# Kernel optimization log

Measured on AMD Instinct MI355X. Metric: run time of the kernel, lower is better.

## Reference

```python
import jax, jax.numpy as jnp
import numpy as np

# Dims
B, C, D, H, W = 2, 64, 16, 64, 64
G = 2            # deformable groups (choose_group(64, 2) -> 2)
K = 27           # 3x3x3 kernel points
GC = C // G      # channels per group
AXIS = (0.5, 1.0, 1.0)   # offset_axis_scale (d, h, w)
EPS = 1e-5
# kernel point offsets for k=3, pad=1, dilation=1: {-1,0,1}^3
_KOFF = np.array([(a, b, c) for a in (-1, 0, 1) for b in (-1, 0, 1) for c in (-1, 0, 1)], dtype=np.float32)


def conv3d(x, w, b=None, pad=0):
    y = jax.lax.conv_general_dilated(x, w, (1, 1, 1), [(pad, pad)] * 3,
                                     dimension_numbers=('NCDHW', 'OIDHW', 'NCDHW'))
    if b is not None:
        y = y + b[None, :, None, None, None]
    return y


def proj1x1(x, w, b=None):
    y = jnp.einsum('oc,bcdhw->bodhw', w, x)
    if b is not None:
        y = y + b[None, :, None, None, None]
    return y


def _trilinear_sample(vflat, pd, ph, pw):
    # vflat: [B,G,GC,DHW]; pd/ph/pw: [B,G,DHW] float sampling coords; zeros padding outside
    d0 = jnp.floor(pd); h0 = jnp.floor(ph); w0 = jnp.floor(pw)
    td, th, tw = pd - d0, ph - h0, pw - w0
    d0 = d0.astype(jnp.int32); h0 = h0.astype(jnp.int32); w0 = w0.astype(jnp.int32)
    acc = jnp.zeros_like(vflat)
    for dd in (0, 1):
        for hh in (0, 1):
            for ww in (0, 1):
                di, hi, wi = d0 + dd, h0 + hh, w0 + ww
                valid = ((di >= 0) & (di < D) & (hi >= 0) & (hi < H) & (wi >= 0) & (wi < W)).astype(vflat.dtype)
                idx = (jnp.clip(di, 0, D - 1) * H + jnp.clip(hi, 0, H - 1)) * W + jnp.clip(wi, 0, W - 1)
                g = jnp.take_along_axis(vflat, jnp.broadcast_to(idx[:, :, None, :], vflat.shape), axis=3)
                wgt = ((td if dd else 1.0 - td) * (th if hh else 1.0 - th) * (tw if ww else 1.0 - tw)) * valid
                acc = acc + g * wgt[:, :, None, :]
    return acc


def setup_inputs() -> dict:
    key = jax.random.key(0)
    ks = jax.random.split(key, 8)
    f = jnp.float32
    s = 1.0 / np.sqrt(C)
    return {
        'x': jax.random.normal(ks[0], (B, C, D, H, W), f),
        'gate': jnp.zeros((), f),
        'pre_w': jax.random.normal(ks[1], (C, C, 1, 1, 1), f) * s,
        'post_w': jax.random.normal(ks[2], (C, C, 1, 1, 1), f) * s,
        'in_proj_w': jax.random.normal(ks[3], (C, C), f) * s,
        'in_proj_b': jnp.zeros((C,), f),
        'out_proj_w': jax.random.normal(ks[4], (C, C), f) * s,
        'out_proj_b': jnp.zeros((C,), f),
        'off_w': jax.random.normal(ks[5], (3 * G * K, C, 3, 3, 3), f) * 0.01,
        'off_b': jnp.zeros((3 * G * K,), f),
        'mask_w': jax.random.normal(ks[6], (G * K, C, 3, 3, 3), f) * 0.01,
        'mask_b': jnp.zeros((G * K,), f),
        'in_gamma': jnp.ones((C,), f),
        'in_beta': jnp.zeros((C,), f),
    }


def reference(x, gate, pre_w, post_w, in_proj_w, in_proj_b, out_proj_w, out_proj_b,
              off_w, off_b, mask_w, mask_b, in_gamma, in_beta):
    DHW = D * H * W
    xp = conv3d(x, pre_w)                                      # pre 1x1
    # --- DCNv3_3D: value projection, learned offsets + softmax modulation mask ---
    v = proj1x1(xp, in_proj_w, in_proj_b).reshape(B, G, GC, DHW)
    off = conv3d(xp, off_w, off_b, pad=1).reshape(B, G, K, 3, DHW)   # warmed-up offset_scale = 1.0
    m = jax.nn.softmax(conv3d(xp, mask_w, mask_b, pad=1).reshape(B, G, K, DHW), axis=2)
    dg, hg, wg = jnp.meshgrid(jnp.arange(D, dtype=jnp.float32),
                              jnp.arange(H, dtype=jnp.float32),
                              jnp.arange(W, dtype=jnp.float32), indexing='ij')
    dg, hg, wg = dg.reshape(-1), hg.reshape(-1), wg.reshape(-1)      # [DHW]
    out = jnp.zeros_like(v)
    for k in range(K):   # fixed small loop over 27 kernel points
        pd = dg + _KOFF[k, 0] + off[:, :, k, 0] * AXIS[0]
        ph = hg + _KOFF[k, 1] + off[:, :, k, 1] * AXIS[1]
        pw = wg + _KOFF[k, 2] + off[:, :, k, 2] * AXIS[2]
        out = out + _trilinear_sample(v, pd, ph, pw) * m[:, :, k, :][:, :, None, :]
    y = out.reshape(B, C, D, H, W)
    y = proj1x1(y, out_proj_w, out_proj_b)
    # InstanceNorm3d + GELU
    mu = y.mean(axis=(2, 3, 4), keepdims=True)
    var = y.var(axis=(2, 3, 4), keepdims=True)
    y = (y - mu) * jax.lax.rsqrt(var + EPS)
    y = y * in_gamma[None, :, None, None, None] + in_beta[None, :, None, None, None]
    y = jax.nn.gelu(y)
    y = conv3d(y, post_w)                                      # post 1x1
    return x + jax.nn.sigmoid(gate) * y
```

## Files before the change

### kernel.cpp

```cpp
#include <hip/hip_runtime.h>
#include <hip/hip_bf16.h>

typedef short short8 __attribute__((ext_vector_type(8)));
typedef float f32x4 __attribute__((ext_vector_type(4)));
typedef _Float16 h2 __attribute__((ext_vector_type(2)));
typedef __fp16 fp16x2 __attribute__((ext_vector_type(2)));

#if __has_builtin(__builtin_elementwise_fma)
#define FMA2H(a, b, c) __builtin_elementwise_fma((a), (b), (c))
#else
#define FMA2H(a, b, c) ((a) * (b) + (c))
#endif

namespace {
constexpr int Bn = 2, Cn = 64, Dn = 16, Hn = 64, Wn = 64;
constexpr int Gn = 2, Kn = 27, GCn = 32;
constexpr int DHW = Dn * Hn * Wn;
constexpr int OCn = 216;
constexpr int PD = 18, PH = 66, PW = 66;
constexpr float EPS = 1e-5f;

constexpr int PROWS = 12 * 66;
constexpr int PATCH_B = PROWS * 128;

constexpr size_t XPADH_OFF = 0;
constexpr size_t XPADH_B   = (size_t)Bn * PD * PH * PW * Cn * 2;
constexpr size_t WFRAG_OFF = XPADH_OFF + XPADH_B;
constexpr size_t WFRAG_B   = (size_t)54 * 16 * 64 * 16;
constexpr size_t WV_OFF    = WFRAG_OFF + WFRAG_B;
constexpr size_t WV_B      = 64 * 64 * 4;
constexpr size_t CONV_OFF  = WV_OFF + WV_B;
constexpr size_t CONV_B    = (size_t)Bn * OCn * DHW * 2;
constexpr size_t V_OFF     = CONV_OFF + CONV_B;
constexpr size_t V_B       = (size_t)Bn * Gn * DHW * GCn * 2;
constexpr size_t SAMP_OFF  = V_OFF + V_B;
constexpr size_t SAMP_B    = (size_t)Bn * Gn * DHW * GCn * 2;
constexpr size_t STAT_OFF  = SAMP_OFF + SAMP_B;
constexpr size_t VBH_OFF   = STAT_OFF + 4096;
constexpr size_t VFRAG_OFF = VBH_OFF + 256;
constexpr size_t OFRAG_OFF = VFRAG_OFF + 8192;
constexpr size_t PFRAG_OFF = OFRAG_OFF + 8192;
}

__device__ inline float b2f(short s) {
  union { float f; unsigned u; } x; x.u = ((unsigned)(unsigned short)s) << 16; return x.f;
}
__device__ inline short f2b(float f) {
  __hip_bfloat16 h = __float2bfloat16(f);
  union { __hip_bfloat16 h; short s; } x; x.h = h; return x.s;
}
__device__ inline int iclamp(int v, int lo, int hi) { return v < lo ? lo : (v > hi ? hi : v); }
__device__ inline h2 u2h2(unsigned u) {
  union { unsigned u; h2 h; } x; x.u = u; return x.h;
}
__device__ inline unsigned h2u(h2 h) {
  union { unsigned u; h2 h; } x; x.h = h; return x.u;
}
__device__ inline h2 pkrtz(float a, float b) {
#if __has_builtin(__builtin_amdgcn_cvt_pkrtz)
  union { fp16x2 p; h2 h; } x;
  x.p = __builtin_amdgcn_cvt_pkrtz(a, b);
  return x.h;
#else
  return (h2){(_Float16)a, (_Float16)b};
#endif
}

__global__ __launch_bounds__(256) void zerofill(uint4* __restrict__ p, int n16) {
  int i = blockIdx.x * 256 + threadIdx.x;
  if (i < n16) p[i] = make_uint4(0, 0, 0, 0);
}

__global__ __launch_bounds__(256) void fillpad(const float* __restrict__ x,
                                               __hip_bfloat16* __restrict__ xpadh) {
  int tid = threadIdx.x;
  int w5 = tid & 31, cq = tid >> 5;
  int p = blockIdx.x * 32 + w5;
  int b = blockIdx.y;
  int w = p & 63, h = (p >> 6) & 63, d = p >> 12;
  const float* xb = x + ((size_t)b * 64 + cq * 8) * DHW + p;
  short8 o8;
#pragma unroll
  for (int j = 0; j < 8; ++j) o8[j] = f2b(xb[(size_t)j * DHW]);
  __hip_bfloat16* ob = xpadh + (size_t)b * (PD * PH * PW * 64)
      + ((((size_t)(d + 1) * 66) + (h + 1)) * 66 + (w + 1)) * 64 + cq * 8;
  *(short8*)ob = o8;
}

__global__ __launch_bounds__(256) void fold_weights(
    const float* __restrict__ pre_w, const float* __restrict__ in_proj_w,
    const float* __restrict__ off_w, const float* __restrict__ mask_w,
    short8* __restrict__ Wfrag, float* __restrict__ Wv) {
  int i = blockIdx.x * 256 + threadIdx.x;
  if (i < 64 * 64) {
    int o = i >> 6, c = i & 63;
    float s = 0.f;
    for (int cp = 0; cp < 64; ++cp) s += in_proj_w[o * 64 + cp] * pre_w[cp * 64 + c];
    Wv[i] = s;
    return;
  }
  int t = i - 64 * 64;
  if (t >= 54 * 16 * 64) return;
  int l = t & 63; int rest = t >> 6;
  int mt = rest & 15; int ks = rest >> 4;
  int oc = mt * 16 + (l & 15);
  int tap = ks >> 1;
  int c0 = (ks & 1) * 32 + (l >> 4) * 8;
  float vals[8] = {0.f, 0.f, 0.f, 0.f, 0.f, 0.f, 0.f, 0.f};
  if (oc < OCn) {
    const float* cw = (oc < 162) ? (off_w + (size_t)oc * 64 * 27)
                                 : (mask_w + (size_t)(oc - 162) * 64 * 27);
#pragma unroll 1
    for (int cp = 0; cp < 64; ++cp) {
      float wv = cw[cp * 27 + tap];
      const float* pr = pre_w + cp * 64 + c0;
#pragma unroll
      for (int j = 0; j < 8; ++j) vals[j] += wv * pr[j];
    }
  }
  short8 o8;
#pragma unroll
  for (int j = 0; j < 8; ++j) o8[j] = f2b(vals[j]);
  Wfrag[t] = o8;
}

__global__ __launch_bounds__(256) void packfrag(
    const float* __restrict__ Wv, const float* __restrict__ Wout,
    const float* __restrict__ Wpost, const float* __restrict__ vb,
    short8* __restrict__ vfrag, short8* __restrict__ ofrag,
    short8* __restrict__ pfrag, h2* __restrict__ vbh) {
  int i = blockIdx.x * 256 + threadIdx.x;
  if (i < 32) vbh[i] = pkrtz(vb[2 * i], vb[2 * i + 1]);
  int which = i >> 9;
  int t = i & 511;
  int l = t & 63, mt = (t >> 6) & 3, ks = t >> 8;
  int m = mt * 16 + (l & 15);
  int k0 = ks * 32 + (l >> 4) * 8;
  const float* W = (which == 0) ? Wv : (which == 1) ? Wout : Wpost;
  short8 o;
#pragma unroll
  for (int j = 0; j < 8; ++j) o[j] = f2b(W[m * 64 + k0 + j]);
  if (which == 0) vfrag[t] = o;
  else if (which == 1) ofrag[t] = o;
  else pfrag[t] = o;
}

#define GEMM_MFMA_BODY(FRAG)                                                  \
  int wid = tid >> 6, l = tid & 63, lm = l & 15, lk = l >> 4;                 \
  f32x4 acc[4][4];                                                            \
  _Pragma("unroll")                                                           \
  for (int mt = 0; mt < 4; ++mt)                                              \
    _Pragma("unroll")                                                         \
    for (int nt = 0; nt < 4; ++nt) acc[mt][nt] = (f32x4){0.f, 0.f, 0.f, 0.f}; \
  _Pragma("unroll")                                                           \
  for (int ks = 0; ks < 2; ++ks) {                                            \
    short8 af[4], bf[4];                                                      \
    _Pragma("unroll")                                                         \
    for (int mt = 0; mt < 4; ++mt) af[mt] = FRAG[(ks * 4 + mt) * 64 + l];     \
    _Pragma("unroll")                                                         \
    for (int nt = 0; nt < 4; ++nt) {                                          \
      int sr = wid * 64 + nt * 16 + lm;                                       \
      int us = ks * 4 + lk;                                                   \
      bf[nt] = *(const short8*)(stg + sr * 128 + ((us ^ (sr & 7)) << 4));     \
    }                                                                         \
    _Pragma("unroll")                                                         \
    for (int mt = 0; mt < 4; ++mt)                                            \
      _Pragma("unroll")                                                       \
      for (int nt = 0; nt < 4; ++nt)                                          \
        acc[mt][nt] = __builtin_amdgcn_mfma_f32_16x16x32_bf16(af[mt], bf[nt], acc[mt][nt], 0, 0, 0); \
  }

__global__ __launch_bounds__(256) void vproj_mfma(
    const char* __restrict__ xpadh, const short8* __restrict__ vfrag,
    const h2* __restrict__ vbh, _Float16* __restrict__ v) {
  __shared__ char stg[32768];
  __shared__ char bnc[256 * 144];
  int tid = threadIdx.x;
  int p0 = blockIdx.x * 256, b = blockIdx.y;
  const char* xb = xpadh + (size_t)b * (PD * PH * PW * 128);
#pragma unroll
  for (int it = 0; it < 8; ++it) {
    int idx = it * 256 + tid;
    int s = idx >> 3, slot = idx & 7;
    int p = p0 + s, w = p & 63, h = (p >> 6) & 63, d = p >> 12;
    const char* g = xb + ((((size_t)(d + 1)) * 66 + (h + 1)) * 66 + (w + 1)) * 128 + slot * 16;
    *(uint4*)(stg + s * 128 + ((slot ^ (s & 7)) << 4)) = *(const uint4*)g;
  }
  __syncthreads();
  GEMM_MFMA_BODY(vfrag)
#pragma unroll
  for (int mt = 0; mt < 4; ++mt)
#pragma unroll
    for (int nt = 0; nt < 4; ++nt)
#pragma unroll
      for (int r = 0; r < 4; ++r) {
        int pos = wid * 64 + nt * 16 + lm;
        int oc = mt * 16 + lk * 4 + r;
        *(_Float16*)(bnc + pos * 144 + oc * 2) = (_Float16)acc[mt][nt][r];
      }
  __syncthreads();
  {
    int p = p0 + tid;
    const unsigned* brow = (const unsigned*)(bnc + tid * 144);
    char* vb0 = (char*)v + ((size_t)(b * 2 + 0) * DHW + p) * 64;
    char* vb1 = (char*)v + ((size_t)(b * 2 + 1) * DHW + p) * 64;
#pragma unroll
    for (int s = 0; s < 8; ++s) {
      uint4 ov;
      unsigned* po = (unsigned*)&ov;
#pragma unroll
      for (int j = 0; j < 4; ++j) {
        h2 hv = u2h2(brow[s * 4 + j]) + vbh[s * 4 + j];
        po[j] = h2u(hv);
      }
      if (s < 4) *(uint4*)(vb0 + s * 16) = ov;
      else       *(uint4*)(vb1 + (s - 4) * 16) = ov;
    }
  }
}

__global__ __launch_bounds__(512) void conv_mfma(
    const char* __restrict__ xpadh, const char* __restrict__ wfrag,
    const float* __restrict__ off_b, const float* __restrict__ mask_b,
    __hip_bfloat16* __restrict__ convout) {
  __shared__ char lds[PATCH_B];
  int tid = threadIdx.x;
  int h0 = blockIdx.x * 2, d = blockIdx.y, b = blockIdx.z;

  const char* xb = xpadh + (size_t)b * (PD * PH * PW * 128);
  for (int idx = tid; idx < PROWS * 8; idx += 512) {
    int s = idx >> 3, slot = idx & 7;
    int r12 = s / 66, wx = s - r12 * 66;
    int dp = r12 >> 2, hp = r12 & 3;
    const char* g = xb + ((((size_t)(d + dp)) * 66 + (h0 + hp)) * 66 + wx) * 128 + slot * 16;
    *(uint4*)(lds + s * 128 + ((slot ^ (s & 7)) << 4)) = *(const uint4*)g;
  }
  __syncthreads();

  int wid = tid >> 6, l = tid & 63;
  int wm = wid & 3, wn = wid >> 2;
  int lm = l & 15, lk = l >> 4;
  const char* abase = wfrag + ((size_t)((wm * 4) * 64 + l)) * 16;

  f32x4 acc[4][4];
#pragma unroll
  for (int mt = 0; mt < 4; ++mt)
#pragma unroll
    for (int nt = 0; nt < 4; ++nt) acc[mt][nt] = (f32x4){0.f, 0.f, 0.f, 0.f};

  short8 A0[4], B0[4], A1[4], B1[4], A2[4], B2[4];

#define LOADA(KS, A)                                                          \
  {                                                                           \
    const char* ap_ = abase + (KS) * 16384;                                   \
    _Pragma("unroll")                                                         \
    for (int mt = 0; mt < 4; ++mt) A[mt] = *(const short8*)(ap_ + mt * 1024); \
  }
#define LOADB(KS, B)                                                          \
  {                                                                           \
    int tap_ = (KS) >> 1;                                                     \
    int dd_ = tap_ / 9, rem_ = tap_ - dd_ * 9;                                \
    int dh_ = rem_ / 3, dw_ = rem_ - dh_ * 3;                                 \
    int srow_ = (dd_ * 4 + wn + dh_) * 66 + dw_;                              \
    int uslot_ = 4 * ((KS) & 1) + lk;                                         \
    _Pragma("unroll")                                                         \
    for (int nt = 0; nt < 4; ++nt) {                                          \
      int sr_ = srow_ + nt * 16 + lm;                                         \
      B[nt] = *(const short8*)(lds + sr_ * 128 + ((uslot_ ^ (sr_ & 7)) << 4)); \
    }                                                                         \
  }
#define MFMAS(A, B)                                                           \
  __builtin_amdgcn_s_setprio(1);                                              \
  _Pragma("unroll")                                                           \
  for (int mt = 0; mt < 4; ++mt)                                              \
    _Pragma("unroll")                                                         \
    for (int nt = 0; nt < 4; ++nt)                                            \
      acc[mt][nt] = __builtin_amdgcn_mfma_f32_16x16x32_bf16(A[mt], B[nt], acc[mt][nt], 0, 0, 0); \
  __builtin_amdgcn_s_setprio(0);

  LOADA(0, A0) LOADB(0, B0)
  LOADA(1, A1) LOADB(1, B1)
#pragma unroll 1
  for (int ks = 0; ks < 54; ks += 3) {
    LOADA(ks + 2, A2) LOADB(ks + 2, B2)
    MFMAS(A0, B0)
    if (ks + 3 < 54) { LOADA(ks + 3, A0) LOADB(ks + 3, B0) }
    MFMAS(A1, B1)
    if (ks + 4 < 54) { LOADA(ks + 4, A1) LOADB(ks + 4, B1) }
    MFMAS(A2, B2)
  }
#undef LOADA
#undef LOADB
#undef MFMAS

  int pbase = d * 4096 + (h0 + wn) * 64;
#pragma unroll
  for (int mt = 0; mt < 4; ++mt) {
    int oc0 = wm * 64 + mt * 16 + lk * 4;
#pragma unroll
    for (int r = 0; r < 4; ++r) {
      int oc = oc0 + r;
      if (oc < OCn) {
        float bias = (oc < 162) ? off_b[oc] : mask_b[oc - 162];
        size_t orow = ((size_t)b * OCn + oc) * DHW + pbase;
#pragma unroll
        for (int nt = 0; nt < 4; ++nt)
          convout[orow + nt * 16 + lm] = __float2bfloat16(acc[mt][nt][r] + bias);
      }
    }
  }
}

__global__ __launch_bounds__(256) void dcn_sample(
    const __hip_bfloat16* __restrict__ convout, const _Float16* __restrict__ v,
    short* __restrict__ sampled) {
  __shared__ short offm[108 * 64];
  int tid = threadIdx.x;
  int id = blockIdx.x;
  int bg = (id & 7) >> 1;
  int p0 = (((id >> 3) << 1) + (id & 1)) * 64;
  int b = bg >> 1, g = bg & 1;

  const __hip_bfloat16* cb = convout + (size_t)b * OCn * DHW;
#pragma unroll 1
  for (int idx = tid; idx < 108 * 8; idx += 256) {
    int row = idx >> 3, col = idx & 7;
    int oc = (row < 81) ? (g * 81 + row) : (162 + g * Kn + (row - 81));
    *(uint4*)(offm + row * 64 + col * 8) = *(const uint4*)(cb + (size_t)oc * DHW + p0 + col * 8);
  }
  __syncthreads();

  int pl = tid >> 2, q = tid & 3;
  int p = p0 + pl;
  int w = p & 63, h = (p >> 6) & 63, d = p >> 12;

  float msum = 0.f;
  h2 acc[4];
#pragma unroll
  for (int j = 0; j < 4; ++j) acc[j] = (h2){(_Float16)0.f, (_Float16)0.f};
  const char* vg = (const char*)v + ((size_t)bg * DHW * GCn + q * 8) * 2;

#pragma unroll 1
  for (int k = 0; k < Kn; ++k) {
    float offd = b2f(offm[(3 * k + 0) * 64 + pl]);
    float offh = b2f(offm[(3 * k + 1) * 64 + pl]);
    float offw = b2f(offm[(3 * k + 2) * 64 + pl]);
    float pd = (float)(d + (k / 9) - 1) + offd * 0.5f;
    float ph = (float)(h + ((k / 3) % 3) - 1) + offh;
    float pw = (float)(w + (k % 3) - 1) + offw;
    float fd = floorf(pd), fh = floorf(ph), fw = floorf(pw);
    float td = pd - fd, th = ph - fh, tw = pw - fw;
    int d0 = (int)fd, h0 = (int)fh, w0 = (int)fw;
    float ek = __expf(b2f(offm[(81 + k) * 64 + pl]));
    msum += ek;

    float wd0 = ((unsigned)d0 < (unsigned)Dn) ? (1.f - td) * ek : 0.f;
    float wd1 = ((unsigned)(d0 + 1) < (unsigned)Dn) ? td * ek : 0.f;
    float wh0 = ((unsigned)h0 < (unsigned)Hn) ? (1.f - th) : 0.f;
    float wh1 = ((unsigned)(h0 + 1) < (unsigned)Hn) ? th : 0.f;
    float ww0 = ((unsigned)w0 < (unsigned)Wn) ? (1.f - tw) : 0.f;
    float ww1 = ((unsigned)(w0 + 1) < (unsigned)Wn) ? tw : 0.f;
    int dr0 = iclamp(d0, 0, Dn - 1) << 18, dr1 = iclamp(d0 + 1, 0, Dn - 1) << 18;
    int hr0 = iclamp(h0, 0, Hn - 1) << 12, hr1 = iclamp(h0 + 1, 0, Hn - 1) << 12;
    int wc0 = iclamp(w0, 0, Wn - 1) << 6,  wc1 = iclamp(w0 + 1, 0, Wn - 1) << 6;
    float wdh00 = wd0 * wh0, wdh01 = wd0 * wh1, wdh10 = wd1 * wh0, wdh11 = wd1 * wh1;

#define CORNER(BOFF, WT)                                                \
    {                                                                   \
      _Float16 wh_ = (_Float16)(WT);                                    \
      h2 w2_ = {wh_, wh_};                                              \
      uint4 u_ = *(const uint4*)(vg + (BOFF));                          \
      acc[0] = FMA2H(u2h2(u_.x), w2_, acc[0]);                          \
      acc[1] = FMA2H(u2h2(u_.y), w2_, acc[1]);                          \
      acc[2] = FMA2H(u2h2(u_.z), w2_, acc[2]);                          \
      acc[3] = FMA2H(u2h2(u_.w), w2_, acc[3]);                          \
    }
    CORNER(dr0 + hr0 + wc0, wdh00 * ww0)
    CORNER(dr0 + hr0 + wc1, wdh00 * ww1)
    CORNER(dr0 + hr1 + wc0, wdh01 * ww0)
    CORNER(dr0 + hr1 + wc1, wdh01 * ww1)
    CORNER(dr1 + hr0 + wc0, wdh10 * ww0)
    CORNER(dr1 + hr0 + wc1, wdh10 * ww1)
    CORNER(dr1 + hr1 + wc0, wdh11 * ww0)
    CORNER(dr1 + hr1 + wc1, wdh11 * ww1)
#undef CORNER
  }

  float rs = 1.f / msum;
  short8 o8;
#pragma unroll
  for (int j = 0; j < 4; ++j) {
    o8[2 * j]     = f2b((float)acc[j][0] * rs);
    o8[2 * j + 1] = f2b((float)acc[j][1] * rs);
  }
  *(short8*)((char*)sampled + ((size_t)bg * DHW + p) * 64 + q * 16) = o8;
}

__global__ __launch_bounds__(256) void outproj_mfma(
    const short* __restrict__ sampled, const short8* __restrict__ ofrag,
    const float* __restrict__ ob, __hip_bfloat16* __restrict__ t) {
  __shared__ char stg[32768];
  __shared__ char bnc[256 * 144];
  int tid = threadIdx.x;
  int p0 = blockIdx.x * 256, b = blockIdx.y;
#pragma unroll
  for (int it = 0; it < 8; ++it) {
    int idx = it * 256 + tid;
    int s = idx >> 3, slot = idx & 7;
    int g = slot >> 2;
    const char* src = (const char*)sampled + ((size_t)(b * 2 + g) * DHW + p0 + s) * 64 + (slot & 3) * 16;
    *(uint4*)(stg + s * 128 + ((slot ^ (s & 7)) << 4)) = *(const uint4*)src;
  }
  __syncthreads();
  GEMM_MFMA_BODY(ofrag)
#pragma unroll
  for (int mt = 0; mt < 4; ++mt)
#pragma unroll
    for (int r = 0; r < 4; ++r) {
      int oc = mt * 16 + lk * 4 + r;
      float bias = ob[oc];
#pragma unroll
      for (int nt = 0; nt < 4; ++nt) {
        int pos = wid * 64 + nt * 16 + lm;
        *(short*)(bnc + pos * 144 + oc * 2) = f2b(acc[mt][nt][r] + bias);
      }
    }
  __syncthreads();
  {
    int c = tid & 63, pq = tid >> 6;
    short* trow = (short*)t + ((size_t)b * 64 + c) * DHW + p0 + pq * 64;
#pragma unroll
    for (int s8 = 0; s8 < 8; ++s8) {
      short8 o8;
#pragma unroll
      for (int j = 0; j < 8; ++j)
        o8[j] = *(const short*)(bnc + (pq * 64 + s8 * 8 + j) * 144 + c * 2);
      *(short8*)(trow + s8 * 8) = o8;
    }
  }
}

__global__ __launch_bounds__(256) void stats_k(const __hip_bfloat16* __restrict__ t,
                                               float* __restrict__ stat) {
  int bc = blockIdx.x;
  const short8* tc = (const short8*)(t + (size_t)bc * DHW);
  float s = 0.f, ss = 0.f;
  for (int i = threadIdx.x; i < DHW / 8; i += 256) {
    short8 s8 = tc[i];
#pragma unroll
    for (int j = 0; j < 8; ++j) { float xv = b2f(s8[j]); s += xv; ss += xv * xv; }
  }
#pragma unroll
  for (int o = 32; o > 0; o >>= 1) { s += __shfl_down(s, o); ss += __shfl_down(ss, o); }
  __shared__ float ls[4], lss[4];
  int wid = threadIdx.x >> 6;
  if ((threadIdx.x & 63) == 0) { ls[wid] = s; lss[wid] = ss; }
  __syncthreads();
  if (threadIdx.x == 0) {
    float S = ls[0] + ls[1] + ls[2] + ls[3];
    float SS = lss[0] + lss[1] + lss[2] + lss[3];
    float mu = S / (float)DHW;
    float var = SS / (float)DHW - mu * mu;
    stat[bc * 2 + 0] = mu;
    stat[bc * 2 + 1] = rsqrtf(var + EPS);
  }
}

__global__ __launch_bounds__(256) void normgelu(
    const __hip_bfloat16* __restrict__ t, const float* __restrict__ stat,
    const float* __restrict__ gamma, const float* __restrict__ beta,
    short* __restrict__ nvh) {
  int p = blockIdx.x * 256 + threadIdx.x;
  int b = blockIdx.y;
  short o[64];
#pragma unroll
  for (int c = 0; c < Cn; ++c) {
    float mu = stat[(b * Cn + c) * 2 + 0];
    float rstd = stat[(b * Cn + c) * 2 + 1];
    float tv = b2f(((const short*)t)[((size_t)b * Cn + c) * DHW + p]);
    float yv = (tv - mu) * rstd * gamma[c] + beta[c];
    float u = 0.7978845608028654f * (yv + 0.044715f * yv * yv * yv);
    float e = __expf(2.f * u);
    float th = 1.f - 2.f / (e + 1.f);
    o[c] = f2b(0.5f * yv * (1.f + th));
  }
  short* dst = nvh + ((size_t)b * DHW + p) * 64;
#pragma unroll
  for (int s8 = 0; s8 < 8; ++s8) {
    short8 o8;
#pragma unroll
    for (int j = 0; j < 8; ++j) o8[j] = o[s8 * 8 + j];
    *(short8*)(dst + s8 * 8) = o8;
  }
}

__global__ __launch_bounds__(256) void post_mfma(
    const short* __restrict__ nvh, const short8* __restrict__ pfrag,
    const float* __restrict__ x, const float* __restrict__ gate,
    float* __restrict__ out) {
  __shared__ char stg[32768];
  __shared__ char bnc[256 * 144];
  int tid = threadIdx.x;
  int p0 = blockIdx.x * 256, b = blockIdx.y;
#pragma unroll
  for (int it = 0; it < 8; ++it) {
    int idx = it * 256 + tid;
    int s = idx >> 3, slot = idx & 7;
    const char* src = (const char*)nvh + ((size_t)b * DHW + p0 + s) * 128 + slot * 16;
    *(uint4*)(stg + s * 128 + ((slot ^ (s & 7)) << 4)) = *(const uint4*)src;
  }
  __syncthreads();
  GEMM_MFMA_BODY(pfrag)
#pragma unroll
  for (int mt = 0; mt < 4; ++mt)
#pragma unroll
    for (int nt = 0; nt < 4; ++nt)
#pragma unroll
      for (int r = 0; r < 4; ++r) {
        int pos = wid * 64 + nt * 16 + lm;
        int oc = mt * 16 + lk * 4 + r;
        *(short*)(bnc + pos * 144 + oc * 2) = f2b(acc[mt][nt][r]);
      }
  __syncthreads();
  {
    float sg = 1.f / (1.f + __expf(-gate[0]));
    int c = tid & 63, pq = tid >> 6;
    size_t base = ((size_t)b * 64 + c) * DHW + p0 + pq * 64;
    const float4* x4 = (const float4*)(x + base);
    float4* o4 = (float4*)(out + base);
#pragma unroll
    for (int qd = 0; qd < 16; ++qd) {
      float4 xv = x4[qd];
      float v0 = b2f(*(const short*)(bnc + (pq * 64 + qd * 4 + 0) * 144 + c * 2));
      float v1 = b2f(*(const short*)(bnc + (pq * 64 + qd * 4 + 1) * 144 + c * 2));
      float v2 = b2f(*(const short*)(bnc + (pq * 64 + qd * 4 + 2) * 144 + c * 2));
      float v3 = b2f(*(const short*)(bnc + (pq * 64 + qd * 4 + 3) * 144 + c * 2));
      o4[qd] = make_float4(xv.x + sg * v0, xv.y + sg * v1, xv.z + sg * v2, xv.w + sg * v3);
    }
  }
}

extern "C" void kernel_launch(void* const* d_in, const int* in_sizes, int n_in,
                              void* d_out, int out_size, void* d_ws, size_t ws_size,
                              hipStream_t stream) {
  const float* x          = (const float*)d_in[0];
  const float* gate       = (const float*)d_in[1];
  const float* pre_w      = (const float*)d_in[2];
  const float* post_w     = (const float*)d_in[3];
  const float* in_proj_w  = (const float*)d_in[4];
  const float* in_proj_b  = (const float*)d_in[5];
  const float* out_proj_w = (const float*)d_in[6];
  const float* out_proj_b = (const float*)d_in[7];
  const float* off_w      = (const float*)d_in[8];
  const float* off_b      = (const float*)d_in[9];
  const float* mask_w     = (const float*)d_in[10];
  const float* mask_b     = (const float*)d_in[11];
  const float* in_gamma   = (const float*)d_in[12];
  const float* in_beta    = (const float*)d_in[13];

  char* ws = (char*)d_ws;
  __hip_bfloat16* xpadh = (__hip_bfloat16*)(ws + XPADH_OFF);
  short8* Wfrag  = (short8*)(ws + WFRAG_OFF);
  float* Wv      = (float*)(ws + WV_OFF);
  __hip_bfloat16* convout = (__hip_bfloat16*)(ws + CONV_OFF);
  _Float16* v    = (_Float16*)(ws + V_OFF);
  short* sampled = (short*)(ws + SAMP_OFF);
  short* nvh     = (short*)(ws + SAMP_OFF);
  float* stat    = (float*)(ws + STAT_OFF);
  h2* vbh        = (h2*)(ws + VBH_OFF);
  short8* vfrag  = (short8*)(ws + VFRAG_OFF);
  short8* ofrag  = (short8*)(ws + OFRAG_OFF);
  short8* pfrag  = (short8*)(ws + PFRAG_OFF);
  __hip_bfloat16* t = (__hip_bfloat16*)(ws + XPADH_OFF);
  float* out = (float*)d_out;

  int zf16 = (int)(XPADH_B / 16);
  zerofill<<<(zf16 + 255) / 256, 256, 0, stream>>>((uint4*)xpadh, zf16);
  fillpad<<<dim3(DHW / 32, Bn), 256, 0, stream>>>(x, xpadh);
  int foldN = (64 * 64 + 54 * 16 * 64 + 255) / 256;
  fold_weights<<<foldN, 256, 0, stream>>>(pre_w, in_proj_w, off_w, mask_w, Wfrag, Wv);
  packfrag<<<6, 256, 0, stream>>>(Wv, out_proj_w, post_w, in_proj_b,
                                  vfrag, ofrag, pfrag, vbh);
  vproj_mfma<<<dim3(DHW / 256, Bn), 256, 0, stream>>>((const char*)xpadh, vfrag, vbh, v);
  conv_mfma<<<dim3(32, 16, 2), 512, 0, stream>>>((const char*)xpadh, (const char*)Wfrag,
                                                 off_b, mask_b, convout);
  dcn_sample<<<4096, 256, 0, stream>>>(convout, v, sampled);
  outproj_mfma<<<dim3(DHW / 256, Bn), 256, 0, stream>>>(sampled, ofrag, out_proj_b, t);
  stats_k<<<Bn * Cn, 256, 0, stream>>>(t, stat);
  normgelu<<<dim3(DHW / 256, Bn), 256, 0, stream>>>(t, stat, in_gamma, in_beta, nvh);
  post_mfma<<<dim3(DHW / 256, Bn), 256, 0, stream>>>(nvh, pfrag, x, gate, out);
}
```

Baseline: 338.9 us.

## Split conv K-loop across wave halves with LDS reduction of partial accumulators

The conv_mfma kernel now gives each wave both output rows (8 N-tiles) but only half of the K-steps (even or odd channel halves per tap), then sums the two partial accumulators through LDS before the bias add and store. This doubles register-level reuse of each A fragment across N-tiles and halves the A loads per wave. The cost is a larger accumulator footprint (128 floats per lane), an extra LDS reduction with several barriers, and a launch-bounds hint of 2 blocks per SM that may force register spills. Pipelining depth drops from triple to double buffering.

```diff
diff --git a/kernel.cpp b/kernel.cpp
--- a/kernel.cpp
+++ b/kernel.cpp
@@ -219,7 +219,7 @@
   }
 }
 
-__global__ __launch_bounds__(512) void conv_mfma(
+__global__ __launch_bounds__(512, 2) void conv_mfma(
     const char* __restrict__ xpadh, const char* __restrict__ wfrag,
     const float* __restrict__ off_b, const float* __restrict__ mask_b,
     __hip_bfloat16* __restrict__ convout) {
@@ -238,17 +238,18 @@
   __syncthreads();
 
   int wid = tid >> 6, l = tid & 63;
-  int wm = wid & 3, wn = wid >> 2;
+  int wm = wid & 3, kh = wid >> 2;
   int lm = l & 15, lk = l >> 4;
   const char* abase = wfrag + ((size_t)((wm * 4) * 64 + l)) * 16;
-
-  f32x4 acc[4][4];
+  int uslot = 4 * kh + lk;
+
+  f32x4 acc[4][8];
 #pragma unroll
   for (int mt = 0; mt < 4; ++mt)
 #pragma unroll
-    for (int nt = 0; nt < 4; ++nt) acc[mt][nt] = (f32x4){0.f, 0.f, 0.f, 0.f};
-
-  short8 A0[4], B0[4], A1[4], B1[4], A2[4], B2[4];
+    for (int nt = 0; nt < 8; ++nt) acc[mt][nt] = (f32x4){0.f, 0.f, 0.f, 0.f};
+
+  short8 A0[4], A1[4], B0[8];
 
 #define LOADA(KS, A)                                                          \
   {                                                                           \
@@ -261,12 +262,10 @@
     int tap_ = (KS) >> 1;                                                     \
     int dd_ = tap_ / 9, rem_ = tap_ - dd_ * 9;                                \
     int dh_ = rem_ / 3, dw_ = rem_ - dh_ * 3;                                 \
-    int srow_ = (dd_ * 4 + wn + dh_) * 66 + dw_;                              \
-    int uslot_ = 4 * ((KS) & 1) + lk;                                         \
     _Pragma("unroll")                                                         \
-    for (int nt = 0; nt < 4; ++nt) {                                          \
-      int sr_ = srow_ + nt * 16 + lm;                                         \
-      B[nt] = *(const short8*)(lds + sr_ * 128 + ((uslot_ ^ (sr_ & 7)) << 4)); \
+    for (int nt = 0; nt < 8; ++nt) {                                          \
+      int sr_ = (dd_ * 4 + (nt >> 2) + dh_) * 66 + dw_ + (nt & 3) * 16 + lm;  \
+      B[nt] = *(const short8*)(lds + sr_ * 128 + ((uslot ^ (sr_ & 7)) << 4)); \
     }                                                                         \
   }
 #define MFMAS(A, B)                                                           \
@@ -274,38 +273,77 @@
   _Pragma("unroll")                                                           \
   for (int mt = 0; mt < 4; ++mt)                                              \
     _Pragma("unroll")                                                         \
-    for (int nt = 0; nt < 4; ++nt)                                            \
+    for (int nt = 0; nt < 8; ++nt)                                            \
       acc[mt][nt] = __builtin_amdgcn_mfma_f32_16x16x32_bf16(A[mt], B[nt], acc[mt][nt], 0, 0, 0); \
   __builtin_amdgcn_s_setprio(0);
 
-  LOADA(0, A0) LOADB(0, B0)
-  LOADA(1, A1) LOADB(1, B1)
+  LOADA(kh, A0)
 #pragma unroll 1
-  for (int ks = 0; ks < 54; ks += 3) {
-    LOADA(ks + 2, A2) LOADB(ks + 2, B2)
+  for (int i = 0; i < 26; i += 2) {
+    LOADA(2 * (i + 1) + kh, A1)
+    LOADB(2 * i + kh, B0)
     MFMAS(A0, B0)
-    if (ks + 3 < 54) { LOADA(ks + 3, A0) LOADB(ks + 3, B0) }
-    MFMAS(A1, B1)
-    if (ks + 4 < 54) { LOADA(ks + 4, A1) LOADB(ks + 4, B1) }
-    MFMAS(A2, B2)
-  }
+    LOADA(2 * (i + 2) + kh, A0)
+    LOADB(2 * (i + 1) + kh, B0)
+    MFMAS(A1, B0)
+  }
+  LOADB(52 + kh, B0)
+  MFMAS(A0, B0)
 #undef LOADA
 #undef LOADB
 #undef MFMAS
 
-  int pbase = d * 4096 + (h0 + wn) * 64;
-#pragma unroll
-  for (int mt = 0; mt < 4; ++mt) {
-    int oc0 = wm * 64 + mt * 16 + lk * 4;
-#pragma unroll
-    for (int r = 0; r < 4; ++r) {
-      int oc = oc0 + r;
-      if (oc < OCn) {
-        float bias = (oc < 162) ? off_b[oc] : mask_b[oc - 162];
-        size_t orow = ((size_t)b * OCn + oc) * DHW + pbase;
-#pragma unroll
-        for (int nt = 0; nt < 4; ++nt)
-          convout[orow + nt * 16 + lm] = __float2bfloat16(acc[mt][nt][r] + bias);
+  __syncthreads();
+  float* red = (float*)lds;
+#pragma unroll
+  for (int ph = 0; ph < 2; ++ph) {
+    if (kh == 1) {
+#pragma unroll
+      for (int mi = 0; mi < 2; ++mi) {
+        int mt = ph * 2 + mi;
+#pragma unroll
+        for (int nt = 0; nt < 8; ++nt)
+#pragma unroll
+          for (int r = 0; r < 4; ++r) {
+            int ocl = mi * 16 + lk * 4 + r;
+            int pos = nt * 16 + lm;
+            red[wm * 4128 + ocl * 129 + pos] = acc[mt][nt][r];
+          }
+      }
+    }
+    __syncthreads();
+    if (kh == 0) {
+#pragma unroll
+      for (int mi = 0; mi < 2; ++mi) {
+        int mt = ph * 2 + mi;
+#pragma unroll
+        for (int nt = 0; nt < 8; ++nt)
+#pragma unroll
+          for (int r = 0; r < 4; ++r) {
+            int ocl = mi * 16 + lk * 4 + r;
+            int pos = nt * 16 + lm;
+            acc[mt][nt][r] += red[wm * 4128 + ocl * 129 + pos];
+          }
+      }
+    }
+    __syncthreads();
+  }
+
+  if (kh == 0) {
+    int pbase = d * 4096 + h0 * 64;
+#pragma unroll
+    for (int mt = 0; mt < 4; ++mt) {
+      int oc0 = wm * 64 + mt * 16 + lk * 4;
+#pragma unroll
+      for (int r = 0; r < 4; ++r) {
+        int oc = oc0 + r;
+        if (oc < OCn) {
+          float bias = (oc < 162) ? off_b[oc] : mask_b[oc - 162];
+          size_t orow = ((size_t)b * OCn + oc) * DHW + pbase;
+#pragma unroll
+          for (int nt = 0; nt < 8; ++nt)
+            convout[orow + nt * 16 + lm] = __float2bfloat16(acc[mt][nt][r] + bias);
+        }
       }
     }
   }
```

Result: slower. 349.2 us (+3.0%).

## Stream conv input one depth slice at a time to shrink LDS and registers

Applied to the files above, without the earlier changes.

The conv_mfma kernel now stages one padded depth slice (4x66 rows) into LDS per outer iteration instead of the full 3-slice patch, cutting shared memory to a third. It also drops the triple-buffered A/B register pipeline for a single buffer and sets launch_bounds min-blocks to 4, aiming for more resident blocks per CU. The cost is extra barriers per block and less software pipelining between loads and MFMAs, so load latency may be exposed.

```diff
diff --git a/kernel.cpp b/kernel.cpp
--- a/kernel.cpp
+++ b/kernel.cpp
@@ -20,8 +20,8 @@
 constexpr int PD = 18, PH = 66, PW = 66;
 constexpr float EPS = 1e-5f;
 
-constexpr int PROWS = 12 * 66;
-constexpr int PATCH_B = PROWS * 128;
+constexpr int SROWS = 4 * 66;
+constexpr int SLICE_B = SROWS * 128;
 
 constexpr size_t XPADH_OFF = 0;
 constexpr size_t XPADH_B   = (size_t)Bn * PD * PH * PW * Cn * 2;
@@ -219,28 +219,19 @@
   }
 }
 
-__global__ __launch_bounds__(512) void conv_mfma(
+__global__ __launch_bounds__(512, 4) void conv_mfma(
     const char* __restrict__ xpadh, const char* __restrict__ wfrag,
     const float* __restrict__ off_b, const float* __restrict__ mask_b,
     __hip_bfloat16* __restrict__ convout) {
-  __shared__ char lds[PATCH_B];
+  __shared__ char lds[SLICE_B];
   int tid = threadIdx.x;
   int h0 = blockIdx.x * 2, d = blockIdx.y, b = blockIdx.z;
-
-  const char* xb = xpadh + (size_t)b * (PD * PH * PW * 128);
-  for (int idx = tid; idx < PROWS * 8; idx += 512) {
-    int s = idx >> 3, slot = idx & 7;
-    int r12 = s / 66, wx = s - r12 * 66;
-    int dp = r12 >> 2, hp = r12 & 3;
-    const char* g = xb + ((((size_t)(d + dp)) * 66 + (h0 + hp)) * 66 + wx) * 128 + slot * 16;
-    *(uint4*)(lds + s * 128 + ((slot ^ (s & 7)) << 4)) = *(const uint4*)g;
-  }
-  __syncthreads();
 
   int wid = tid >> 6, l = tid & 63;
   int wm = wid & 3, wn = wid >> 2;
   int lm = l & 15, lk = l >> 4;
   const char* abase = wfrag + ((size_t)((wm * 4) * 64 + l)) * 16;
+  const char* xb = xpadh + (size_t)b * (PD * PH * PW * 128);
 
   f32x4 acc[4][4];
 #pragma unroll
@@ -248,50 +239,56 @@
 #pragma unroll
     for (int nt = 0; nt < 4; ++nt) acc[mt][nt] = (f32x4){0.f, 0.f, 0.f, 0.f};
 
-  short8 A0[4], B0[4], A1[4], B1[4], A2[4], B2[4];
-
-#define LOADA(KS, A)                                                          \
+  short8 A0[4], B0[4];
+
+#define LOADA(KS)                                                             \
   {                                                                           \
     const char* ap_ = abase + (KS) * 16384;                                   \
     _Pragma("unroll")                                                         \
-    for (int mt = 0; mt < 4; ++mt) A[mt] = *(const short8*)(ap_ + mt * 1024); \
-  }
-#define LOADB(KS, B)                                                          \
-  {                                                                           \
-    int tap_ = (KS) >> 1;                                                     \
-    int dd_ = tap_ / 9, rem_ = tap_ - dd_ * 9;                                \
-    int dh_ = rem_ / 3, dw_ = rem_ - dh_ * 3;                                 \
-    int srow_ = (dd_ * 4 + wn + dh_) * 66 + dw_;                              \
-    int uslot_ = 4 * ((KS) & 1) + lk;                                         \
-    _Pragma("unroll")                                                         \
-    for (int nt = 0; nt < 4; ++nt) {                                          \
-      int sr_ = srow_ + nt * 16 + lm;                                         \
-      B[nt] = *(const short8*)(lds + sr_ * 128 + ((uslot_ ^ (sr_ & 7)) << 4)); \
-    }                                                                         \
-  }
-#define MFMAS(A, B)                                                           \
-  __builtin_amdgcn_s_setprio(1);                                              \
-  _Pragma("unroll")                                                           \
-  for (int mt = 0; mt < 4; ++mt)                                              \
-    _Pragma("unroll")                                                         \
-    for (int nt = 0; nt < 4; ++nt)                                            \
-      acc[mt][nt] = __builtin_amdgcn_mfma_f32_16x16x32_bf16(A[mt], B[nt], acc[mt][nt], 0, 0, 0); \
-  __builtin_amdgcn_s_setprio(0);
-
-  LOADA(0, A0) LOADB(0, B0)
-  LOADA(1, A1) LOADB(1, B1)
+    for (int mt = 0; mt < 4; ++mt) A0[mt] = *(const short8*)(ap_ + mt * 1024); \
+  }
+  LOADA(0)
+
 #pragma unroll 1
-  for (int ks = 0; ks < 54; ks += 3) {
-    LOADA(ks + 2, A2) LOADB(ks + 2, B2)
-    MFMAS(A0, B0)
-    if (ks + 3 < 54) { LOADA(ks + 3, A0) LOADB(ks + 3, B0) }
-    MFMAS(A1, B1)
-    if (ks + 4 < 54) { LOADA(ks + 4, A1) LOADB(ks + 4, B1) }
-    MFMAS(A2, B2)
+  for (int dd = 0; dd < 3; ++dd) {
+    __syncthreads();
+#pragma unroll
+    for (int it = 0; it < 5; ++it) {
+      int idx = it * 512 + tid;
+      if (idx < SROWS * 8) {
+        int s = idx >> 3, slot = idx & 7;
+        int hp = s / 66, wx = s - hp * 66;
+        const char* g = xb + ((((size_t)(d + dd)) * 66 + (h0 + hp)) * 66 + wx) * 128 + slot * 16;
+        *(uint4*)(lds + s * 128 + ((slot ^ (s & 7)) << 4)) = *(const uint4*)g;
+      }
+    }
+    __syncthreads();
+
+#pragma unroll 1
+    for (int tl = 0; tl < 9; ++tl) {
+      int dh = tl / 3, dw = tl - dh * 3;
+      int srow = (wn + dh) * 66 + dw;
+#pragma unroll
+      for (int ch = 0; ch < 2; ++ch) {
+        int ks = dd * 18 + tl * 2 + ch;
+        int uslot = 4 * ch + lk;
+#pragma unroll
+        for (int nt = 0; nt < 4; ++nt) {
+          int sr = srow + nt * 16 + lm;
+          B0[nt] = *(const short8*)(lds + sr * 128 + ((uslot ^ (sr & 7)) << 4));
+        }
+        __builtin_amdgcn_s_setprio(1);
+#pragma unroll
+        for (int mt = 0; mt < 4; ++mt)
+#pragma unroll
+          for (int nt = 0; nt < 4; ++nt)
+            acc[mt][nt] = __builtin_amdgcn_mfma_f32_16x16x32_bf16(A0[mt], B0[nt], acc[mt][nt], 0, 0, 0);
+        __builtin_amdgcn_s_setprio(0);
+        if (ks + 1 < 54) LOADA(ks + 1)
+      }
+    }
   }
 #undef LOADA
-#undef LOADB
-#undef MFMAS
 
   int pbase = d * 4096 + (h0 + wn) * 64;
 #pragma unroll
```

Measured after the change: 328.1 us. 3.2% less time.
